# Kernel tuning notes

Measured on AMD Instinct MI355X. Metric: run time of the kernel, lower is better.

The kernel has to match this reference:

```python
import jax, jax.numpy as jnp
import numpy as np


def setup_inputs() -> dict:
    key = jax.random.key(0)
    k1, k2 = jax.random.split(key)
    B, S, D = 4, 2048, 1024
    x = jax.random.normal(k1, (B, S, D), dtype=jnp.float32)
    # uniform initializer in keras is small; scale to keep softmax well-behaved
    kernel = jax.random.normal(k2, (3, D, D), dtype=jnp.float32) * 0.02
    return {"x": x, "kernel": kernel}


def reference(x, kernel):
    # x: [B, S, D], kernel: [3, D, D]
    D = x.shape[-1]
    q = jnp.einsum('bsd,de->bse', x, kernel[0])
    k = jnp.einsum('bsd,de->bse', x, kernel[1])
    v = jnp.einsum('bsd,de->bse', x, kernel[2])
    scores = jnp.einsum('bqe,bke->bqk', q, k) / jnp.sqrt(jnp.float32(D))
    attn = jax.nn.softmax(scores, axis=-1)
    return jnp.einsum('bqk,bke->bqe', attn, v)
```

## Files before the change

### kernel.cpp

```cpp
#include <hip/hip_runtime.h>
#include <hip/hip_bf16.h>
#include <cstdint>

typedef __bf16 bf16x8 __attribute__((ext_vector_type(8)));
typedef float f32x4 __attribute__((ext_vector_type(4)));

__device__ __forceinline__ unsigned short f2bf(float f) {
  union { float f; uint32_t u; } a; a.f = f;
  uint32_t r = a.u + 0x7fffu + ((a.u >> 16) & 1u);
  return (unsigned short)(r >> 16);
}
__device__ __forceinline__ uint32_t pk2(float lo, float hi) {
  return (uint32_t)f2bf(lo) | ((uint32_t)f2bf(hi) << 16);
}
__device__ __forceinline__ void gload_lds16(const unsigned short* g, unsigned short* l) {
  __builtin_amdgcn_global_load_lds(
      (const __attribute__((address_space(1))) void*)g,
      (__attribute__((address_space(3))) void*)l, 16, 0, 0);
}

__global__ void cast_w(const float* __restrict__ W, unsigned short* __restrict__ Wt) {
  __shared__ float tileW[64][65];
  const int b = blockIdx.x;
  const int t = threadIdx.x;
  const int z = b >> 8;
  const int rest = b & 255;
  const int bxx = rest & 15, byy = rest >> 4;
  const float* Wz = W + (size_t)z * 1048576;
  unsigned short* Wtz = Wt + (size_t)z * 1048576;
  const int x0 = bxx * 64, y0 = byy * 64;
  {
    const int r = t >> 4;
    const int c = (t & 15) * 4;
#pragma unroll
    for (int p = 0; p < 64; p += 16) {
      float4 v = *(const float4*)(Wz + (size_t)(y0 + p + r) * 1024 + x0 + c);
      tileW[p + r][c + 0] = v.x;
      tileW[p + r][c + 1] = v.y;
      tileW[p + r][c + 2] = v.z;
      tileW[p + r][c + 3] = v.w;
    }
  }
  __syncthreads();
  {
    const int dc = (t & 7) * 8;
#pragma unroll
    for (int p = 0; p < 64; p += 32) {
      const int e = p + (t >> 3);
      uint4 o;
      o.x = pk2(tileW[dc + 0][e], tileW[dc + 1][e]);
      o.y = pk2(tileW[dc + 2][e], tileW[dc + 3][e]);
      o.z = pk2(tileW[dc + 4][e], tileW[dc + 5][e]);
      o.w = pk2(tileW[dc + 6][e], tileW[dc + 7][e]);
      *(uint4*)(Wtz + (size_t)(x0 + e) * 1024 + y0 + dc) = o;
    }
  }
}

__global__ void reduce_aux(const float* __restrict__ partial, float* __restrict__ rowinv) {
  const int r = blockIdx.x * 256 + threadIdx.x;
  float s = 0.f;
#pragma unroll
  for (int j = 0; j < 32; ++j) s += partial[(size_t)j * 8192 + r];
  rowinv[r] = 1.f / s;
}

__global__ void __launch_bounds__(256)
gemm_qkv(const float* __restrict__ X, const unsigned short* __restrict__ Wtall,
         unsigned short* __restrict__ QK, unsigned short* __restrict__ Vt) {
  __shared__ unsigned short As[2][4096];
  __shared__ unsigned short Bs[2][4096];
  const int t = threadIdx.x;
  const int lane = t & 63;
  const int quad = lane >> 4;
  const int l15 = lane & 15;
  const int wave = t >> 6;
  const int wm = (wave >> 1) * 64;
  const int wn = (wave & 1) * 64;
  const int z = blockIdx.z;

  const unsigned short* Bt = Wtall + (size_t)z * 1048576 + (size_t)blockIdx.y * 131072;

  const int srow = t >> 2;
  const int scol = (((t & 3) ^ ((srow >> 1) & 3)) * 8);
  const float* gx = X + (size_t)(blockIdx.x * 128 + srow) * 1024 + scol;
  const unsigned short* gb = Bt + (size_t)srow * 1024 + scol;

  const int aOff = (wm + l15) * 32 + (quad ^ ((l15 >> 1) & 3)) * 8;
  const int bOff = (wn + l15) * 32 + (quad ^ ((l15 >> 1) & 3)) * 8;

  f32x4 acc[4][4];
#pragma unroll
  for (int i = 0; i < 4; i++)
#pragma unroll
    for (int j = 0; j < 4; j++) acc[i][j] = (f32x4){0.f, 0.f, 0.f, 0.f};

  float4 ar0, ar1, ar2, ar3;
#define LOADA(KN) do {                                        \
    ar0 = *(const float4*)(gx + (KN));                        \
    ar1 = *(const float4*)(gx + (KN) + 4);                    \
    ar2 = *(const float4*)(gx + 65536 + (KN));                \
    ar3 = *(const float4*)(gx + 65536 + (KN) + 4);            \
  } while (0)

  LOADA(0);
  gload_lds16(gb, &Bs[0][t * 8]);
  gload_lds16(gb + 65536, &Bs[0][2048 + t * 8]);

  int buf = 0;
  for (int k0 = 0; k0 < 1024; k0 += 32, buf ^= 1) {
    uint4 w0, w1;
    w0.x = pk2(ar0.x, ar0.y); w0.y = pk2(ar0.z, ar0.w);
    w0.z = pk2(ar1.x, ar1.y); w0.w = pk2(ar1.z, ar1.w);
    w1.x = pk2(ar2.x, ar2.y); w1.y = pk2(ar2.z, ar2.w);
    w1.z = pk2(ar3.x, ar3.y); w1.w = pk2(ar3.z, ar3.w);
    *(uint4*)(&As[buf][t * 8]) = w0;
    *(uint4*)(&As[buf][2048 + t * 8]) = w1;
    __syncthreads();
    if (k0 + 32 < 1024) {
      const int kn = k0 + 32;
      LOADA(kn);
      gload_lds16(gb + kn, &Bs[buf ^ 1][t * 8]);
      gload_lds16(gb + 65536 + kn, &Bs[buf ^ 1][2048 + t * 8]);
    }
    const unsigned short* aB = &As[buf][aOff];
    const unsigned short* bB = &Bs[buf][bOff];
    bf16x8 a[4], b[4];
#pragma unroll
    for (int i = 0; i < 4; i++) a[i] = *(const bf16x8*)(aB + i * 512);
#pragma unroll
    for (int j = 0; j < 4; j++) b[j] = *(const bf16x8*)(bB + j * 512);
#pragma unroll
    for (int i = 0; i < 4; i++)
#pragma unroll
      for (int j = 0; j < 4; j++)
        acc[i][j] = __builtin_amdgcn_mfma_f32_16x16x32_bf16(a[i], b[j], acc[i][j], 0, 0, 0);
  }
#undef LOADA

  const int mbase = blockIdx.x * 128 + wm + quad * 4;
  const int nbase = blockIdx.y * 128 + wn + l15;

  if (z < 2) {
    unsigned short* C = QK + (size_t)z * 8388608;
#pragma unroll
    for (int mi = 0; mi < 4; mi++)
#pragma unroll
      for (int ni = 0; ni < 4; ni++) {
        const int m = mbase + mi * 16, n = nbase + ni * 16;
#pragma unroll
        for (int r = 0; r < 4; r++)
          C[(size_t)(m + r) * 1024 + n] = f2bf(acc[mi][ni][r]);
      }
  } else {
#pragma unroll
    for (int mi = 0; mi < 4; mi++) {
      const int m = mbase + mi * 16;
      const int b = m >> 11, s = m & 2047;
#pragma unroll
      for (int ni = 0; ni < 4; ni++) {
        const int n = nbase + ni * 16;
        uint2 val;
        val.x = pk2(acc[mi][ni][0], acc[mi][ni][1]);
        val.y = pk2(acc[mi][ni][2], acc[mi][ni][3]);
        *(uint2*)(Vt + (size_t)b * 2097152 + (size_t)n * 2048 + s) = val;
      }
    }
  }
}

__global__ void __launch_bounds__(512, 2)
gemm8_scores(const unsigned short* __restrict__ Aall,
             const unsigned short* __restrict__ Btall,
             unsigned short* __restrict__ Call, float* __restrict__ aux,
             int K, int ldc, long sA, long sB, long sC, float scale) {
  __shared__ unsigned short As[2][2][8192];
  __shared__ unsigned short Bs[2][2][8192];
  const int t = threadIdx.x;
  const int lane = t & 63;
  const int quad = lane >> 4;
  const int l15 = lane & 15;
  const int wave = t >> 6;
  const int wm = wave >> 2;
  const int wn = wave & 3;
  const int z = blockIdx.z;
  const int NT = K >> 6;

  const unsigned short* Ab = Aall + (size_t)z * sA + (size_t)blockIdx.x * 256 * K;
  const unsigned short* Bb = Btall + (size_t)z * sB + (size_t)blockIdx.y * 256 * K;

  const int sc = (((t & 3) ^ ((t >> 3) & 3)) * 8);
  const unsigned short* gA = Ab + (size_t)(t >> 2) * K + sc;
  const unsigned short* gB = Bb + (size_t)(t >> 2) * K + sc;
  const size_t half2 = (size_t)128 * K;

  const int swz = (quad ^ ((l15 >> 1) & 3)) * 8;
  const int aRd = (wm * 128 + l15) * 32 + swz;
  const int bRd = (wn * 64 + l15) * 32 + swz;

  f32x4 acc[8][4];
#pragma unroll
  for (int i = 0; i < 8; ++i)
#pragma unroll
    for (int j = 0; j < 4; ++j) acc[i][j] = (f32x4){0.f, 0.f, 0.f, 0.f};

#define STG_A(TT, KH) do { \
    const unsigned short* g_ = gA + (TT) * 64 + (KH) * 32; \
    unsigned short* d_ = &As[(TT) & 1][KH][t * 8]; \
    gload_lds16(g_, d_); \
    gload_lds16(g_ + half2, d_ + 4096); \
  } while (0)
#define STG_B(TT, KH) do { \
    const unsigned short* g_ = gB + (TT) * 64 + (KH) * 32; \
    unsigned short* d_ = &Bs[(TT) & 1][KH][t * 8]; \
    gload_lds16(g_, d_); \
    gload_lds16(g_ + half2, d_ + 4096); \
  } while (0)
#define PHASE_OPEN() do { \
    __builtin_amdgcn_sched_barrier(0); \
    __builtin_amdgcn_s_barrier(); \
    asm volatile("s_waitcnt lgkmcnt(0)" ::: "memory"); \
    __builtin_amdgcn_sched_barrier(0); \
    __builtin_amdgcn_s_setprio(1); \
  } while (0)
#define PHASE_CLOSE() do { \
    __builtin_amdgcn_s_setprio(0); \
    __builtin_amdgcn_sched_barrier(0); \
    __builtin_amdgcn_s_barrier(); \
  } while (0)

  STG_B(0, 0); STG_A(0, 0); STG_B(0, 1); STG_A(0, 1);
  STG_B(1, 0); STG_A(1, 0); STG_B(1, 1);
  asm volatile("s_waitcnt vmcnt(6)" ::: "memory");
  __builtin_amdgcn_s_barrier();

  for (int kt = 0; kt < NT; ++kt) {
    const int buf = kt & 1;
    bf16x8 bb[4], a[4];

#pragma unroll
    for (int j = 0; j < 4; ++j) bb[j] = *(const bf16x8*)&Bs[buf][0][bRd + j * 512];
#pragma unroll
    for (int i = 0; i < 4; ++i) a[i] = *(const bf16x8*)&As[buf][0][aRd + i * 512];
    if (kt + 1 < NT) STG_A(kt + 1, 1);
    PHASE_OPEN();
#pragma unroll
    for (int i = 0; i < 4; ++i)
#pragma unroll
      for (int j = 0; j < 4; ++j)
        acc[i][j] = __builtin_amdgcn_mfma_f32_16x16x32_bf16(a[i], bb[j], acc[i][j], 0, 0, 0);
    PHASE_CLOSE();

#pragma unroll
    for (int i = 0; i < 4; ++i) a[i] = *(const bf16x8*)&As[buf][0][aRd + 2048 + i * 512];
    if (kt + 2 < NT) STG_B(kt + 2, 0);
    PHASE_OPEN();
#pragma unroll
    for (int i = 0; i < 4; ++i)
#pragma unroll
      for (int j = 0; j < 4; ++j)
        acc[4 + i][j] = __builtin_amdgcn_mfma_f32_16x16x32_bf16(a[i], bb[j], acc[4 + i][j], 0, 0, 0);
    PHASE_CLOSE();

#pragma unroll
    for (int j = 0; j < 4; ++j) bb[j] = *(const bf16x8*)&Bs[buf][1][bRd + j * 512];
#pragma unroll
    for (int i = 0; i < 4; ++i) a[i] = *(const bf16x8*)&As[buf][1][aRd + i * 512];
    if (kt + 2 < NT) STG_A(kt + 2, 0);
    PHASE_OPEN();
#pragma unroll
    for (int i = 0; i < 4; ++i)
#pragma unroll
      for (int j = 0; j < 4; ++j)
        acc[i][j] = __builtin_amdgcn_mfma_f32_16x16x32_bf16(a[i], bb[j], acc[i][j], 0, 0, 0);
    PHASE_CLOSE();

#pragma unroll
    for (int i = 0; i < 4; ++i) a[i] = *(const bf16x8*)&As[buf][1][aRd + 2048 + i * 512];
    if (kt + 2 < NT) STG_B(kt + 2, 1);
    __builtin_amdgcn_sched_barrier(0);
    __builtin_amdgcn_s_barrier();
    asm volatile("s_waitcnt lgkmcnt(0)" ::: "memory");
    __builtin_amdgcn_sched_barrier(0);
    __builtin_amdgcn_s_setprio(1);
#pragma unroll
    for (int i = 0; i < 4; ++i)
#pragma unroll
      for (int j = 0; j < 4; ++j)
        acc[4 + i][j] = __builtin_amdgcn_mfma_f32_16x16x32_bf16(a[i], bb[j], acc[4 + i][j], 0, 0, 0);
    __builtin_amdgcn_s_setprio(0);
    __builtin_amdgcn_sched_barrier(0);
    if (kt < NT - 2) {
      asm volatile("s_waitcnt vmcnt(6)" ::: "memory");
    } else if (kt == NT - 2) {
      asm volatile("s_waitcnt vmcnt(0)" ::: "memory");
    }
    __builtin_amdgcn_s_barrier();
  }
#undef STG_A
#undef STG_B

  const int mb = blockIdx.x * 256 + wm * 128 + quad * 4;
  const int nb = blockIdx.y * 256 + wn * 64 + l15;
  const int j = blockIdx.y * 4 + wn;
#pragma unroll
  for (int mi = 0; mi < 8; ++mi) {
#pragma unroll
    for (int r = 0; r < 4; ++r) {
      const int m = mb + mi * 16 + r;
      float s = 0.f;
#pragma unroll
      for (int ni = 0; ni < 4; ++ni) {
        const float e = __expf(acc[mi][ni][r] * scale);
        Call[(size_t)z * sC + (size_t)m * ldc + nb + ni * 16] = f2bf(e);
        s += e;
      }
      s += __shfl_xor(s, 1);
      s += __shfl_xor(s, 2);
      s += __shfl_xor(s, 4);
      s += __shfl_xor(s, 8);
      if (l15 == 0) aux[(size_t)j * 8192 + (size_t)z * 2048 + m] = s;
    }
  }
}

__global__ void __launch_bounds__(512, 2)
gemm8_pv(const unsigned short* __restrict__ Aall,
         const unsigned short* __restrict__ Btall,
         float* __restrict__ Call, const float* __restrict__ rowinv) {
  const int K = 2048, NT = 32;
  __shared__ unsigned short As[2][2][4096];
  __shared__ unsigned short Bs[2][2][8192];
  const int t = threadIdx.x;
  const int lane = t & 63;
  const int quad = lane >> 4;
  const int l15 = lane & 15;
  const int wave = t >> 6;
  const int wm = wave >> 2;
  const int wn = wave & 3;
  const int z = blockIdx.z;

  const unsigned short* Ab = Aall + (size_t)z * 4194304 + (size_t)blockIdx.x * 128 * K;
  const unsigned short* Bb = Btall + (size_t)z * 2097152 + (size_t)blockIdx.y * 256 * K;

  const int sc = (((t & 3) ^ ((t >> 3) & 3)) * 8);
  const unsigned short* gA = Ab + (size_t)(t >> 2) * K + sc;
  const unsigned short* gB = Bb + (size_t)(t >> 2) * K + sc;
  const size_t bhalf = (size_t)128 * K;

  const int swz = (quad ^ ((l15 >> 1) & 3)) * 8;
  const int aRd = (wm * 64 + l15) * 32 + swz;
  const int bRd = (wn * 64 + l15) * 32 + swz;

  f32x4 acc[4][4];
#pragma unroll
  for (int i = 0; i < 4; ++i)
#pragma unroll
    for (int j = 0; j < 4; ++j) acc[i][j] = (f32x4){0.f, 0.f, 0.f, 0.f};

#define STGA(TT, KH) gload_lds16(gA + (TT) * 64 + (KH) * 32, &As[(TT) & 1][KH][t * 8])
#define STGB(TT, KH) do { \
    const unsigned short* g_ = gB + (TT) * 64 + (KH) * 32; \
    unsigned short* d_ = &Bs[(TT) & 1][KH][t * 8]; \
    gload_lds16(g_, d_); \
    gload_lds16(g_ + bhalf, d_ + 4096); \
  } while (0)

  STGB(0, 0); STGA(0, 0); STGB(0, 1); STGA(0, 1);
  STGB(1, 0); STGA(1, 0);
  asm volatile("s_waitcnt vmcnt(3)" ::: "memory");
  __builtin_amdgcn_s_barrier();

  for (int kt = 0; kt < NT; ++kt) {
    const int buf = kt & 1;
    bf16x8 bb[4], a[4];

#pragma unroll
    for (int j = 0; j < 4; ++j) bb[j] = *(const bf16x8*)&Bs[buf][0][bRd + j * 512];
#pragma unroll
    for (int i = 0; i < 4; ++i) a[i] = *(const bf16x8*)&As[buf][0][aRd + i * 512];
    if (kt + 1 < NT) { STGB(kt + 1, 1); STGA(kt + 1, 1); }
    PHASE_OPEN();
#pragma unroll
    for (int i = 0; i < 4; ++i)
#pragma unroll
      for (int j = 0; j < 4; ++j)
        acc[i][j] = __builtin_amdgcn_mfma_f32_16x16x32_bf16(a[i], bb[j], acc[i][j], 0, 0, 0);
    PHASE_CLOSE();

#pragma unroll
    for (int j = 0; j < 4; ++j) bb[j] = *(const bf16x8*)&Bs[buf][1][bRd + j * 512];
#pragma unroll
    for (int i = 0; i < 4; ++i) a[i] = *(const bf16x8*)&As[buf][1][aRd + i * 512];
    if (kt + 2 < NT) { STGB(kt + 2, 0); STGA(kt + 2, 0); }
    __builtin_amdgcn_sched_barrier(0);
    __builtin_amdgcn_s_barrier();
    asm volatile("s_waitcnt lgkmcnt(0)" ::: "memory");
    __builtin_amdgcn_sched_barrier(0);
    __builtin_amdgcn_s_setprio(1);
#pragma unroll
    for (int i = 0; i < 4; ++i)
#pragma unroll
      for (int j = 0; j < 4; ++j)
        acc[i][j] = __builtin_amdgcn_mfma_f32_16x16x32_bf16(a[i], bb[j], acc[i][j], 0, 0, 0);
    __builtin_amdgcn_s_setprio(0);
    __builtin_amdgcn_sched_barrier(0);
    if (kt < NT - 2) {
      asm volatile("s_waitcnt vmcnt(3)" ::: "memory");
    } else if (kt == NT - 2) {
      asm volatile("s_waitcnt vmcnt(0)" ::: "memory");
    }
    __builtin_amdgcn_s_barrier();
  }
#undef STGA
#undef STGB
#undef PHASE_OPEN
#undef PHASE_CLOSE

  const int mb = blockIdx.x * 128 + wm * 64 + quad * 4;
  const int nb = blockIdx.y * 256 + wn * 64 + l15;
#pragma unroll
  for (int mi = 0; mi < 4; ++mi) {
#pragma unroll
    for (int r = 0; r < 4; ++r) {
      const int m = mb + mi * 16 + r;
      const float inv = rowinv[(size_t)z * 2048 + m];
#pragma unroll
      for (int ni = 0; ni < 4; ++ni)
        Call[(size_t)z * 2097152 + (size_t)m * 1024 + nb + ni * 16] = acc[mi][ni][r] * inv;
    }
  }
}

extern "C" void kernel_launch(void* const* d_in, const int* in_sizes, int n_in,
                              void* d_out, int out_size, void* d_ws, size_t ws_size,
                              hipStream_t stream) {
  const float* x = (const float*)d_in[0];
  const float* W = (const float*)d_in[1];
  float* out = (float*)d_out;
  char* ws = (char*)d_ws;
  unsigned short* Wt = (unsigned short*)(ws + (16ll << 20));
  float* partial     = (float*)(ws + (16ll << 20));
  float* rowinv      = (float*)(ws + (18ll << 20));
  unsigned short* Q  = (unsigned short*)(ws + (22ll << 20));
  unsigned short* Kb = (unsigned short*)(ws + (38ll << 20));
  unsigned short* Vt = (unsigned short*)(ws + (54ll << 20));
  unsigned short* Sb = (unsigned short*)(ws + (70ll << 20));
  (void)Kb;

  cast_w<<<768, 256, 0, stream>>>(W, Wt);

  gemm_qkv<<<dim3(64, 8, 3), 256, 0, stream>>>(x, Wt, Q, Vt);

  gemm8_scores<<<dim3(8, 8, 4), 512, 0, stream>>>(
      Q, Q + 8388608, Sb, partial, 1024, 2048, 2097152L, 2097152L, 4194304L, 0.03125f);

  reduce_aux<<<32, 256, 0, stream>>>(partial, rowinv);

  gemm8_pv<<<dim3(16, 4, 4), 512, 0, stream>>>(Sb, Vt, out, rowinv);
}
```

Baseline: 250.9 us.

## Pre-cast x to bf16 and fold row-sum reduction into PV GEMM

Adds a combined cast kernel that converts x to bf16 alongside the weight transpose, so the QKV GEMM can stage A tiles with async global-to-LDS loads instead of fp32 register loads plus in-loop conversion. The separate reduce_aux kernel is removed; each PV block now sums the softmax partials for its 128 rows in its prologue and keeps the inverses in LDS. This trades an extra pass over x and a 16MB bf16 write for halved A traffic and simpler GEMM loops, and removes one launch.

```diff
diff --git a/kernel.cpp b/kernel.cpp
--- a/kernel.cpp
+++ b/kernel.cpp
@@ -19,55 +19,63 @@
       (__attribute__((address_space(3))) void*)l, 16, 0, 0);
 }
 
-__global__ void cast_w(const float* __restrict__ W, unsigned short* __restrict__ Wt) {
+__global__ void cast_all(const float* __restrict__ x, const float* __restrict__ W,
+                         unsigned short* __restrict__ xb, unsigned short* __restrict__ Wt) {
   __shared__ float tileW[64][65];
-  const int b = blockIdx.x;
+  const int bx = blockIdx.x;
   const int t = threadIdx.x;
-  const int z = b >> 8;
-  const int rest = b & 255;
-  const int bxx = rest & 15, byy = rest >> 4;
-  const float* Wz = W + (size_t)z * 1048576;
-  unsigned short* Wtz = Wt + (size_t)z * 1048576;
-  const int x0 = bxx * 64, y0 = byy * 64;
-  {
-    const int r = t >> 4;
-    const int c = (t & 15) * 4;
-#pragma unroll
-    for (int p = 0; p < 64; p += 16) {
-      float4 v = *(const float4*)(Wz + (size_t)(y0 + p + r) * 1024 + x0 + c);
-      tileW[p + r][c + 0] = v.x;
-      tileW[p + r][c + 1] = v.y;
-      tileW[p + r][c + 2] = v.z;
-      tileW[p + r][c + 3] = v.w;
-    }
-  }
-  __syncthreads();
-  {
-    const int dc = (t & 7) * 8;
-#pragma unroll
-    for (int p = 0; p < 64; p += 32) {
-      const int e = p + (t >> 3);
-      uint4 o;
-      o.x = pk2(tileW[dc + 0][e], tileW[dc + 1][e]);
-      o.y = pk2(tileW[dc + 2][e], tileW[dc + 3][e]);
-      o.z = pk2(tileW[dc + 4][e], tileW[dc + 5][e]);
-      o.w = pk2(tileW[dc + 6][e], tileW[dc + 7][e]);
-      *(uint4*)(Wtz + (size_t)(x0 + e) * 1024 + y0 + dc) = o;
-    }
-  }
-}
-
-__global__ void reduce_aux(const float* __restrict__ partial, float* __restrict__ rowinv) {
-  const int r = blockIdx.x * 256 + threadIdx.x;
-  float s = 0.f;
-#pragma unroll
-  for (int j = 0; j < 32; ++j) s += partial[(size_t)j * 8192 + r];
-  rowinv[r] = 1.f / s;
+  if (bx < 4096) {
+    size_t i = ((size_t)bx * 256 + t) * 8;
+    float4 a = *(const float4*)(x + i);
+    float4 b = *(const float4*)(x + i + 4);
+    uint4 o;
+    o.x = pk2(a.x, a.y);
+    o.y = pk2(a.z, a.w);
+    o.z = pk2(b.x, b.y);
+    o.w = pk2(b.z, b.w);
+    *(uint4*)(xb + i) = o;
+  } else {
+    const int b = bx - 4096;
+    const int z = b >> 8;
+    const int rest = b & 255;
+    const int bxx = rest & 15, byy = rest >> 4;
+    const float* Wz = W + (size_t)z * 1048576;
+    unsigned short* Wtz = Wt + (size_t)z * 1048576;
+    const int x0 = bxx * 64, y0 = byy * 64;
+    {
+      const int r = t >> 4;
+      const int c = (t & 15) * 4;
+#pragma unroll
+      for (int p = 0; p < 64; p += 16) {
+        float4 v = *(const float4*)(Wz + (size_t)(y0 + p + r) * 1024 + x0 + c);
+        tileW[p + r][c + 0] = v.x;
+        tileW[p + r][c + 1] = v.y;
+        tileW[p + r][c + 2] = v.z;
+        tileW[p + r][c + 3] = v.w;
+      }
+    }
+    __syncthreads();
+    {
+      const int dc = (t & 7) * 8;
+#pragma unroll
+      for (int p = 0; p < 64; p += 32) {
+        const int e = p + (t >> 3);
+        uint4 o;
+        o.x = pk2(tileW[dc + 0][e], tileW[dc + 1][e]);
+        o.y = pk2(tileW[dc + 2][e], tileW[dc + 3][e]);
+        o.z = pk2(tileW[dc + 4][e], tileW[dc + 5][e]);
+        o.w = pk2(tileW[dc + 6][e], tileW[dc + 7][e]);
+        *(uint4*)(Wtz + (size_t)(x0 + e) * 1024 + y0 + dc) = o;
+      }
+    }
+  }
 }
 
 __global__ void __launch_bounds__(256)
-gemm_qkv(const float* __restrict__ X, const unsigned short* __restrict__ Wtall,
+gemm_qkv(const unsigned short* __restrict__ Aall,
+         const unsigned short* __restrict__ Btall,
          unsigned short* __restrict__ QK, unsigned short* __restrict__ Vt) {
+  const int K = 1024;
   __shared__ unsigned short As[2][4096];
   __shared__ unsigned short Bs[2][4096];
   const int t = threadIdx.x;
@@ -79,12 +87,14 @@
   const int wn = (wave & 1) * 64;
   const int z = blockIdx.z;
 
-  const unsigned short* Bt = Wtall + (size_t)z * 1048576 + (size_t)blockIdx.y * 131072;
+  const unsigned short* A = Aall + (size_t)blockIdx.x * 128 * K;
+  const unsigned short* Bt = Btall + (size_t)z * 1048576 + (size_t)blockIdx.y * 128 * K;
 
   const int srow = t >> 2;
   const int scol = (((t & 3) ^ ((srow >> 1) & 3)) * 8);
-  const float* gx = X + (size_t)(blockIdx.x * 128 + srow) * 1024 + scol;
-  const unsigned short* gb = Bt + (size_t)srow * 1024 + scol;
+  const unsigned short* ga = A + (size_t)srow * K + scol;
+  const unsigned short* gb = Bt + (size_t)srow * K + scol;
+  const size_t rowskip = (size_t)64 * K;
 
   const int aOff = (wm + l15) * 32 + (quad ^ ((l15 >> 1) & 3)) * 8;
   const int bOff = (wn + l15) * 32 + (quad ^ ((l15 >> 1) & 3)) * 8;
@@ -95,33 +105,20 @@
 #pragma unroll
     for (int j = 0; j < 4; j++) acc[i][j] = (f32x4){0.f, 0.f, 0.f, 0.f};
 
-  float4 ar0, ar1, ar2, ar3;
-#define LOADA(KN) do {                                        \
-    ar0 = *(const float4*)(gx + (KN));                        \
-    ar1 = *(const float4*)(gx + (KN) + 4);                    \
-    ar2 = *(const float4*)(gx + 65536 + (KN));                \
-    ar3 = *(const float4*)(gx + 65536 + (KN) + 4);            \
-  } while (0)
-
-  LOADA(0);
+  gload_lds16(ga, &As[0][t * 8]);
+  gload_lds16(ga + rowskip, &As[0][2048 + t * 8]);
   gload_lds16(gb, &Bs[0][t * 8]);
-  gload_lds16(gb + 65536, &Bs[0][2048 + t * 8]);
+  gload_lds16(gb + rowskip, &Bs[0][2048 + t * 8]);
 
   int buf = 0;
-  for (int k0 = 0; k0 < 1024; k0 += 32, buf ^= 1) {
-    uint4 w0, w1;
-    w0.x = pk2(ar0.x, ar0.y); w0.y = pk2(ar0.z, ar0.w);
-    w0.z = pk2(ar1.x, ar1.y); w0.w = pk2(ar1.z, ar1.w);
-    w1.x = pk2(ar2.x, ar2.y); w1.y = pk2(ar2.z, ar2.w);
-    w1.z = pk2(ar3.x, ar3.y); w1.w = pk2(ar3.z, ar3.w);
-    *(uint4*)(&As[buf][t * 8]) = w0;
-    *(uint4*)(&As[buf][2048 + t * 8]) = w1;
+  for (int k0 = 0; k0 < K; k0 += 32, buf ^= 1) {
     __syncthreads();
-    if (k0 + 32 < 1024) {
+    if (k0 + 32 < K) {
       const int kn = k0 + 32;
-      LOADA(kn);
+      gload_lds16(ga + kn, &As[buf ^ 1][t * 8]);
+      gload_lds16(ga + rowskip + kn, &As[buf ^ 1][2048 + t * 8]);
       gload_lds16(gb + kn, &Bs[buf ^ 1][t * 8]);
-      gload_lds16(gb + 65536 + kn, &Bs[buf ^ 1][2048 + t * 8]);
+      gload_lds16(gb + rowskip + kn, &Bs[buf ^ 1][2048 + t * 8]);
     }
     const unsigned short* aB = &As[buf][aOff];
     const unsigned short* bB = &Bs[buf][bOff];
@@ -136,7 +133,6 @@
       for (int j = 0; j < 4; j++)
         acc[i][j] = __builtin_amdgcn_mfma_f32_16x16x32_bf16(a[i], b[j], acc[i][j], 0, 0, 0);
   }
-#undef LOADA
 
   const int mbase = blockIdx.x * 128 + wm + quad * 4;
   const int nbase = blockIdx.y * 128 + wn + l15;
@@ -168,6 +164,19 @@
     }
   }
 }
+
+#define PHASE_OPEN() do { \
+    __builtin_amdgcn_sched_barrier(0); \
+    __builtin_amdgcn_s_barrier(); \
+    asm volatile("s_waitcnt lgkmcnt(0)" ::: "memory"); \
+    __builtin_amdgcn_sched_barrier(0); \
+    __builtin_amdgcn_s_setprio(1); \
+  } while (0)
+#define PHASE_CLOSE() do { \
+    __builtin_amdgcn_s_setprio(0); \
+    __builtin_amdgcn_sched_barrier(0); \
+    __builtin_amdgcn_s_barrier(); \
+  } while (0)
 
 __global__ void __launch_bounds__(512, 2)
 gemm8_scores(const unsigned short* __restrict__ Aall,
@@ -216,18 +225,6 @@
     gload_lds16(g_, d_); \
     gload_lds16(g_ + half2, d_ + 4096); \
   } while (0)
-#define PHASE_OPEN() do { \
-    __builtin_amdgcn_sched_barrier(0); \
-    __builtin_amdgcn_s_barrier(); \
-    asm volatile("s_waitcnt lgkmcnt(0)" ::: "memory"); \
-    __builtin_amdgcn_sched_barrier(0); \
-    __builtin_amdgcn_s_setprio(1); \
-  } while (0)
-#define PHASE_CLOSE() do { \
-    __builtin_amdgcn_s_setprio(0); \
-    __builtin_amdgcn_sched_barrier(0); \
-    __builtin_amdgcn_s_barrier(); \
-  } while (0)
 
   STG_B(0, 0); STG_A(0, 0); STG_B(0, 1); STG_A(0, 1);
   STG_B(1, 0); STG_A(1, 0); STG_B(1, 1);
@@ -327,10 +324,11 @@
 __global__ void __launch_bounds__(512, 2)
 gemm8_pv(const unsigned short* __restrict__ Aall,
          const unsigned short* __restrict__ Btall,
-         float* __restrict__ Call, const float* __restrict__ rowinv) {
+         float* __restrict__ Call, const float* __restrict__ partial) {
   const int K = 2048, NT = 32;
   __shared__ unsigned short As[2][2][4096];
   __shared__ unsigned short Bs[2][2][8192];
+  __shared__ float lds_inv[128];
   const int t = threadIdx.x;
   const int lane = t & 63;
   const int quad = lane >> 4;
@@ -340,6 +338,15 @@
   const int wn = wave & 3;
   const int z = blockIdx.z;
 
+  if (t < 128) {
+    const float* pp = partial + (size_t)z * 2048 + blockIdx.x * 128 + t;
+    float s = 0.f;
+#pragma unroll
+    for (int j = 0; j < 32; ++j) s += pp[(size_t)j * 8192];
+    lds_inv[t] = 1.f / s;
+  }
+  asm volatile("" ::: "memory");
+
   const unsigned short* Ab = Aall + (size_t)z * 4194304 + (size_t)blockIdx.x * 128 * K;
   const unsigned short* Bb = Btall + (size_t)z * 2097152 + (size_t)blockIdx.y * 256 * K;
 
@@ -414,17 +421,16 @@
   }
 #undef STGA
 #undef STGB
-#undef PHASE_OPEN
-#undef PHASE_CLOSE
-
-  const int mb = blockIdx.x * 128 + wm * 64 + quad * 4;
+
+  const int rb = wm * 64 + quad * 4;
+  const int mb = blockIdx.x * 128 + rb;
   const int nb = blockIdx.y * 256 + wn * 64 + l15;
 #pragma unroll
   for (int mi = 0; mi < 4; ++mi) {
 #pragma unroll
     for (int r = 0; r < 4; ++r) {
       const int m = mb + mi * 16 + r;
-      const float inv = rowinv[(size_t)z * 2048 + m];
+      const float inv = lds_inv[rb + mi * 16 + r];
 #pragma unroll
       for (int ni = 0; ni < 4; ++ni)
         Call[(size_t)z * 2097152 + (size_t)m * 1024 + nb + ni * 16] = acc[mi][ni][r] * inv;
@@ -439,23 +445,19 @@
   const float* W = (const float*)d_in[1];
   float* out = (float*)d_out;
   char* ws = (char*)d_ws;
+  unsigned short* xb = (unsigned short*)(ws);
   unsigned short* Wt = (unsigned short*)(ws + (16ll << 20));
   float* partial     = (float*)(ws + (16ll << 20));
-  float* rowinv      = (float*)(ws + (18ll << 20));
   unsigned short* Q  = (unsigned short*)(ws + (22ll << 20));
-  unsigned short* Kb = (unsigned short*)(ws + (38ll << 20));
   unsigned short* Vt = (unsigned short*)(ws + (54ll << 20));
   unsigned short* Sb = (unsigned short*)(ws + (70ll << 20));
-  (void)Kb;
-
-  cast_w<<<768, 256, 0, stream>>>(W, Wt);
-
-  gemm_qkv<<<dim3(64, 8, 3), 256, 0, stream>>>(x, Wt, Q, Vt);
+
+  cast_all<<<4864, 256, 0, stream>>>(x, W, xb, Wt);
+
+  gemm_qkv<<<dim3(64, 8, 3), 256, 0, stream>>>(xb, Wt, Q, Vt);
 
   gemm8_scores<<<dim3(8, 8, 4), 512, 0, stream>>>(
       Q, Q + 8388608, Sb, partial, 1024, 2048, 2097152L, 2097152L, 4194304L, 0.03125f);
 
-  reduce_aux<<<32, 256, 0, stream>>>(partial, rowinv);
-
-  gemm8_pv<<<dim3(16, 4, 4), 512, 0, stream>>>(Sb, Vt, out, rowinv);
-}
+  gemm8_pv<<<dim3(16, 4, 4), 512, 0, stream>>>(Sb, Vt, out, partial);
+}
```

Result: faster. 238.5 us (-4.9%).
